# Performance work log

Hardware: AMD Instinct MI355X
Metric: run time of the kernel (lower is better)

Reference implementation:

```python
import jax, jax.numpy as jnp
import numpy as np
from jax import lax

B, IN_C, OUT_C, K, Z_DIM, H, W = 32, 128, 128, 3, 64, 96, 96
PAD = K // 2


def setup_inputs() -> dict:
    key = jax.random.key(0)
    k1, k2, k3, k4, k5, k6 = jax.random.split(key, 6)
    fan = (2.0 / (IN_C * K * K)) ** 0.5
    x = jax.random.normal(k1, (B, IN_C, H, W), dtype=jnp.float32)
    z = jax.random.normal(k2, (B, Z_DIM), dtype=jnp.float32)
    base_weight = jax.random.normal(k3, (OUT_C, IN_C, K, K), dtype=jnp.float32) * fan
    # torch nn.Linear weights are [out_features, in_features]
    gate_weight = jax.random.normal(k4, (OUT_C, Z_DIM), dtype=jnp.float32) * (1.0 / Z_DIM ** 0.5)
    pw_weight = jax.random.normal(k5, (OUT_C * IN_C, Z_DIM), dtype=jnp.float32) * (1.0 / Z_DIM ** 0.5)
    dw_weight = jax.random.normal(k6, (OUT_C * K * K, Z_DIM), dtype=jnp.float32) * (1.0 / Z_DIM ** 0.5)
    return {"x": x, "z": z, "base_weight": base_weight, "gate_weight": gate_weight,
            "pw_weight": pw_weight, "dw_weight": dw_weight}


def _merged_weight(z, base_weight, gate_weight, pw_weight, dw_weight):
    # BaseOp.get_weight: base * gate(z)  -> [B, out_c, in_c, k, k]
    gate = z @ gate_weight.T                       # [B, out_c]
    w_base = base_weight[None] * gate[:, :, None, None, None]
    # PWOp.get_weight (groups=1): [B, out_c, in_c, 1, 1]
    pw = (z @ pw_weight.T).reshape(B, OUT_C, IN_C)
    # DWOp.get_weight: [B, out_c, 1, k, k]
    dw = (z @ dw_weight.T).reshape(B, OUT_C, 1, K, K)
    # delta = pw * dw broadcast -> [B, out_c, in_c, k, k]
    delta = pw[:, :, :, None, None] * dw
    return w_base + delta


def _per_sample_conv(xi, wi):
    # xi: [in_c, H, W], wi: [out_c, in_c, k, k]
    return lax.conv_general_dilated(
        xi[None], wi, window_strides=(1, 1),
        padding=((PAD, PAD), (PAD, PAD)),
        dimension_numbers=("NCHW", "OIHW", "NCHW"))[0]


def reference(x, z, base_weight, gate_weight, pw_weight, dw_weight):
    w = _merged_weight(z, base_weight, gate_weight, pw_weight, dw_weight)
    return jax.vmap(_per_sample_conv)(x, w)  # [B, out_c, H, W]
```

## Files before the change

kernel.cpp:

```cpp
#include <hip/hip_runtime.h>
#include <hip/hip_bf16.h>

typedef __bf16 bf16x8 __attribute__((ext_vector_type(8)));
typedef float f32x4 __attribute__((ext_vector_type(4)));

__device__ __forceinline__ int swz(int n, int k) {
  int pair = n >> 1;
  int s = (((n & 1) << 2) | k) ^ (pair & 7);
  return (pair << 7) + (s << 4);
}

__device__ __forceinline__ void load_lds16(const void* g, void* l) {
  __builtin_amdgcn_global_load_lds((const __attribute__((address_space(1))) void*)g,
                                   (__attribute__((address_space(3))) void*)l, 16, 0, 0);
}

__global__ __launch_bounds__(512) void prep_kernel(
    const float* __restrict__ x, const float* __restrict__ z,
    const float* __restrict__ gw, const float* __restrict__ pww,
    const float* __restrict__ dww, const float* __restrict__ base,
    __hip_bfloat16* __restrict__ xn, __hip_bfloat16* __restrict__ Wt) {
  __shared__ float tile[128][97];
  int gid = blockIdx.x;
  int tid = threadIdx.x;

  if (gid < 3072) {
    int h = gid % 96;
    int b = gid / 96;
    const float* src = x + (size_t)b * 128 * 9216 + h * 96;
    for (int f = tid; f < 3072; f += 512) {
      int ic = f / 24, w4 = f - ic * 24;
      float4 v = *(const float4*)(src + (size_t)ic * 9216 + w4 * 4);
      tile[ic][w4 * 4 + 0] = v.x; tile[ic][w4 * 4 + 1] = v.y;
      tile[ic][w4 * 4 + 2] = v.z; tile[ic][w4 * 4 + 3] = v.w;
    }
    __syncthreads();
    __hip_bfloat16* bb  = xn + (size_t)b * 4 * 307328;
    __hip_bfloat16* dst = bb + (h + 1) * 3136 + 32;
    for (int o = tid; o < 1536; o += 512) {
      int grp = o / 384, rem = o - grp * 384;
      int w = rem >> 2, chunk = rem & 3;
      __hip_bfloat16 tmp[8];
      #pragma unroll
      for (int e = 0; e < 8; e++) tmp[e] = __float2bfloat16(tile[grp * 32 + chunk * 8 + e][w]);
      *(uint4*)(dst + (size_t)grp * 307328 + w * 32 + chunk * 8) = *(uint4*)tmp;
    }
    if (tid < 32) {
      int u = tid;
      int grp = u >> 3, rem = u & 7;
      int pw = (rem >> 2) ? 97 : 0, k = rem & 3;
      *(uint4*)(bb + (size_t)grp * 307328 + ((h + 1) * 98 + pw) * 32 + k * 8) = make_uint4(0, 0, 0, 0);
    }
    if (h == 0 || h == 95) {
      int ph = (h == 0) ? 0 : 97;
      for (int u = tid; u < 1568; u += 512) {
        int grp = u / 392, rem = u - grp * 392;
        int pw = rem >> 2, k = rem & 3;
        *(uint4*)(bb + (size_t)grp * 307328 + (ph * 98 + pw) * 32 + k * 8) = make_uint4(0, 0, 0, 0);
      }
    }
  } else {
    float* zs  = &tile[0][0];
    float (*res)[5] = (float (*)[5])(&tile[0][0] + 256);
    int pw = gid - 3072;
    int oc = pw & 127;
    int b0 = (pw >> 7) * 4;
    if (tid < 256) zs[tid] = z[b0 * 64 + tid];
    __syncthreads();
    int row = tid;
    if (row < 138) {
      const float* wrow = (row == 0) ? gw + (size_t)oc * 64
                        : (row < 10) ? dww + ((size_t)oc * 9 + (row - 1)) * 64
                                     : pww + ((size_t)oc * 128 + (row - 10)) * 64;
      float wr[64];
      #pragma unroll
      for (int i = 0; i < 16; i++) {
        float4 v = ((const float4*)wrow)[i];
        wr[4*i] = v.x; wr[4*i+1] = v.y; wr[4*i+2] = v.z; wr[4*i+3] = v.w;
      }
      #pragma unroll
      for (int bb = 0; bb < 4; bb++) {
        float a = 0.f;
        #pragma unroll
        for (int i = 0; i < 64; i++) a += zs[bb * 64 + i] * wr[i];
        res[row][bb] = a;
      }
    }
    __syncthreads();
    for (int e = tid; e < 2304; e += 512) {
      int icp = e & 15;
      int r1 = e >> 4;
      int tap = r1 % 9, gb = r1 / 9;
      int grp = gb & 3, bb = gb >> 2;
      int b = b0 + bb;
      int ic = grp * 32 + icp * 2;
      float g = res[0][bb], d = res[1 + tap][bb];
      float p0 = res[10 + ic][bb], p1 = res[11 + ic][bb];
      const float* bp = base + ((size_t)(oc * 128 + ic)) * 9 + tap;
      __hip_bfloat162 o2 = {__float2bfloat16(bp[0] * g + p0 * d),
                            __float2bfloat16(bp[9] * g + p1 * d)};
      *(__hip_bfloat162*)(Wt + ((((size_t)(b * 4 + grp)) * 9 + tap) * 128 + oc) * 32 + icp * 2) = o2;
    }
  }
}

__global__ __launch_bounds__(256, 3) void conv_kernel(
    const __hip_bfloat16* __restrict__ xn, const __hip_bfloat16* __restrict__ Wt,
    float* __restrict__ out) {
  __shared__ __align__(16) char smem[49152];
  char* const xt  = smem;
  char* const wb0 = smem + 24576;
  char* const wb1 = smem + 36864;

  int bid = blockIdx.x;
  int X = bid & 7, q = bid >> 3;
  int logical = X * 288 + q;
  int b   = logical / 72;
  int rem = logical - b * 72;
  int ocg = rem & 1;
  int t36 = rem >> 1;
  int hr  = t36 / 3;
  int wc  = t36 - hr * 3;
  int h0 = hr * 8, w0 = wc * 32;

  int tid = threadIdx.x;
  int lane = tid & 63, wid = tid >> 6;
  int l15 = lane & 15, lk = lane >> 4;

  int xoff[6];
  #pragma unroll
  for (int j = 0; j < 6; j++) {
    int p = j * 256 + tid; if (p > 1359) p = 1359;
    int pair = p >> 3, v = (p & 7) ^ (pair & 7);
    int n = (pair << 1) | (v >> 2), k = v & 3;
    int hh = n / 34, ww = n - hh * 34;
    xoff[j] = ((h0 + hh) * 98 + (w0 + ww)) * 32 + k * 8;
  }
  int wsoff[3];
  #pragma unroll
  for (int i = 0; i < 3; i++) {
    int p = i * 256 + tid;
    int pair = p >> 3, v = (p & 7) ^ (pair & 7);
    int n = (pair << 1) | (v >> 2), k = v & 3;
    int dx = n >> 6, ocl = n & 63;
    wsoff[i] = (dx * 128 + ocg * 64 + ocl) * 32 + k * 8;
  }

  const __hip_bfloat16* xbase = xn + (size_t)b * 4 * 307328;
  const __hip_bfloat16* wbase = Wt + (size_t)b * 147456;

  f32x4 acc[4][4];
  #pragma unroll
  for (int i = 0; i < 4; i++)
    #pragma unroll
    for (int j = 0; j < 4; j++) acc[i][j] = (f32x4){0.f, 0.f, 0.f, 0.f};

  #pragma unroll
  for (int i = 0; i < 3; i++)
    load_lds16(wbase + wsoff[i], wb0 + ((i * 256 + wid * 64) << 4));
  #pragma unroll
  for (int j = 0; j < 6; j++)
    load_lds16(xbase + xoff[j], xt + ((j * 256 + wid * 64) << 4));

#define PHASE(G, T, WCUR, WNXT, DOX, DOW, VM)                                      \
  {                                                                                \
    __builtin_amdgcn_s_barrier();                                                  \
    if (DOX) {                                                                     \
      const __hip_bfloat16* xsrc = xbase + (size_t)(G) * 307328;                   \
      _Pragma("unroll")                                                            \
      for (int j = 0; j < 6; j++)                                                  \
        load_lds16(xsrc + xoff[j], xt + ((j * 256 + wid * 64) << 4));              \
    }                                                                              \
    if (DOW) {                                                                     \
      const __hip_bfloat16* wsrc = wbase + (size_t)((G) * 9 + (T) * 3 + 3) * 4096; \
      _Pragma("unroll")                                                            \
      for (int i = 0; i < 3; i++)                                                  \
        load_lds16(wsrc + wsoff[i], (WNXT) + ((i * 256 + wid * 64) << 4));         \
    }                                                                              \
    asm volatile("s_waitcnt vmcnt(" #VM ")" ::: "memory");                         \
    __builtin_amdgcn_s_barrier();                                                  \
    _Pragma("unroll")                                                              \
    for (int dx = 0; dx < 3; dx++) {                                               \
      bf16x8 bfr[4], afr[4];                                                       \
      _Pragma("unroll")                                                            \
      for (int j = 0; j < 4; j++)                                                  \
        bfr[j] = *(const bf16x8*)((WCUR) + swz(dx * 64 + j * 16 + l15, lk));       \
      _Pragma("unroll")                                                            \
      for (int i = 0; i < 4; i++) {                                                \
        int r = wid * 2 + (i >> 1) + (T);                                          \
        int c = ((i & 1) << 4) + l15 + dx;                                         \
        afr[i] = *(const bf16x8*)(xt + swz(r * 34 + c, lk));                       \
      }                                                                            \
      _Pragma("unroll")                                                            \
      for (int i = 0; i < 4; i++)                                                  \
        _Pragma("unroll")                                                          \
        for (int j = 0; j < 4; j++)                                                \
          acc[i][j] = __builtin_amdgcn_mfma_f32_16x16x32_bf16(afr[i], bfr[j],      \
                                                              acc[i][j], 0, 0, 0); \
    }                                                                              \
  }

  PHASE(0, 0, wb0, wb1, 0, 1, 3)
  PHASE(0, 1, wb1, wb0, 0, 1, 3)
  PHASE(0, 2, wb0, wb1, 0, 1, 3)
  PHASE(1, 0, wb1, wb0, 1, 1, 3)
  PHASE(1, 1, wb0, wb1, 0, 1, 3)
  PHASE(1, 2, wb1, wb0, 0, 1, 3)
  PHASE(2, 0, wb0, wb1, 1, 1, 3)
  PHASE(2, 1, wb1, wb0, 0, 1, 3)
  PHASE(2, 2, wb0, wb1, 0, 1, 3)
  PHASE(3, 0, wb1, wb0, 1, 1, 3)
  PHASE(3, 1, wb0, wb1, 0, 1, 3)
  PHASE(3, 2, wb1, wb0, 0, 0, 0)
#undef PHASE

  float* ob = out + ((size_t)b * 128 + ocg * 64) * 9216;
  #pragma unroll
  for (int j = 0; j < 4; j++) {
    int oc = j * 16 + l15;
    float* op = ob + (size_t)oc * 9216 + h0 * 96 + w0 + lk * 4;
    #pragma unroll
    for (int i = 0; i < 4; i++) {
      int m0 = wid * 64 + i * 16;
      *(f32x4*)(op + (m0 >> 5) * 96 + (m0 & 31)) = acc[i][j];
    }
  }
}

extern "C" void kernel_launch(void* const* d_in, const int* in_sizes, int n_in,
                              void* d_out, int out_size, void* d_ws, size_t ws_size,
                              hipStream_t stream) {
  const float* x   = (const float*)d_in[0];
  const float* z   = (const float*)d_in[1];
  const float* bw  = (const float*)d_in[2];
  const float* gw  = (const float*)d_in[3];
  const float* pww = (const float*)d_in[4];
  const float* dww = (const float*)d_in[5];
  float* out = (float*)d_out;

  char* ws = (char*)d_ws;
  __hip_bfloat16* xn = (__hip_bfloat16*)ws;
  __hip_bfloat16* Wt = (__hip_bfloat16*)(ws + 78675968);

  hipLaunchKernelGGL(prep_kernel, dim3(4096), dim3(512), 0, stream,
                     x, z, gw, pww, dww, bw, xn, Wt);
  hipLaunchKernelGGL(conv_kernel, dim3(2304), dim3(256), 0, stream, xn, Wt, out);
}
```

Before: 138.9 us.

## Reorder conv taps by column to reuse input fragments across row taps

Changes the weight layout written by the prep kernel so that taps are ordered column-major (dx outer, dy inner). The conv kernel's per-phase inner loop now iterates over dy. It loads 8 input A-fragments once per phase and reuses them across the three row taps, instead of reloading 4 fragments for each of three column shifts (12 LDS reads down to 8 per phase). This costs more registers for the fragment array, which may pressure occupancy under the 3-blocks launch bound.

```diff
diff --git a/kernel.cpp b/kernel.cpp
--- a/kernel.cpp
+++ b/kernel.cpp
@@ -94,12 +94,13 @@
       int grp = gb & 3, bb = gb >> 2;
       int b = b0 + bb;
       int ic = grp * 32 + icp * 2;
+      int dy = tap / 3, dx = tap - dy * 3;
       float g = res[0][bb], d = res[1 + tap][bb];
       float p0 = res[10 + ic][bb], p1 = res[11 + ic][bb];
       const float* bp = base + ((size_t)(oc * 128 + ic)) * 9 + tap;
       __hip_bfloat162 o2 = {__float2bfloat16(bp[0] * g + p0 * d),
                             __float2bfloat16(bp[9] * g + p1 * d)};
-      *(__hip_bfloat162*)(Wt + ((((size_t)(b * 4 + grp)) * 9 + tap) * 128 + oc) * 32 + icp * 2) = o2;
+      *(__hip_bfloat162*)(Wt + ((((size_t)(b * 4 + grp)) * 9 + dx * 3 + dy) * 128 + oc) * 32 + icp * 2) = o2;
     }
   }
 }
@@ -142,8 +143,8 @@
     int p = i * 256 + tid;
     int pair = p >> 3, v = (p & 7) ^ (pair & 7);
     int n = (pair << 1) | (v >> 2), k = v & 3;
-    int dx = n >> 6, ocl = n & 63;
-    wsoff[i] = (dx * 128 + ocg * 64 + ocl) * 32 + k * 8;
+    int dy = n >> 6, ocl = n & 63;
+    wsoff[i] = (dy * 128 + ocg * 64 + ocl) * 32 + k * 8;
   }
 
   const __hip_bfloat16* xbase = xn + (size_t)b * 4 * 307328;
@@ -162,7 +163,7 @@
   for (int j = 0; j < 6; j++)
     load_lds16(xbase + xoff[j], xt + ((j * 256 + wid * 64) << 4));
 
-#define PHASE(G, T, WCUR, WNXT, DOX, DOW, VM)                                      \
+#define PHASE(G, DX, WCUR, WNXT, DOX, DOW, VM)                                     \
   {                                                                                \
     __builtin_amdgcn_s_barrier();                                                  \
     if (DOX) {                                                                     \
@@ -172,31 +173,32 @@
         load_lds16(xsrc + xoff[j], xt + ((j * 256 + wid * 64) << 4));              \
     }                                                                              \
     if (DOW) {                                                                     \
-      const __hip_bfloat16* wsrc = wbase + (size_t)((G) * 9 + (T) * 3 + 3) * 4096; \
+      const __hip_bfloat16* wsrc = wbase + (size_t)((G) * 9 + (DX) * 3 + 3) * 4096;\
       _Pragma("unroll")                                                            \
       for (int i = 0; i < 3; i++)                                                  \
         load_lds16(wsrc + wsoff[i], (WNXT) + ((i * 256 + wid * 64) << 4));         \
     }                                                                              \
     asm volatile("s_waitcnt vmcnt(" #VM ")" ::: "memory");                         \
     __builtin_amdgcn_s_barrier();                                                  \
+    bf16x8 afr[4][2];                                                              \
     _Pragma("unroll")                                                              \
-    for (int dx = 0; dx < 3; dx++) {                                               \
-      bf16x8 bfr[4], afr[4];                                                       \
+    for (int rr = 0; rr < 4; rr++)                                                 \
+      _Pragma("unroll")                                                            \
+      for (int cc = 0; cc < 2; cc++)                                               \
+        afr[rr][cc] = *(const bf16x8*)(xt +                                        \
+            swz((wid * 2 + rr) * 34 + cc * 16 + l15 + (DX), lk));                  \
+    _Pragma("unroll")                                                              \
+    for (int dy = 0; dy < 3; dy++) {                                               \
+      bf16x8 bfr[4];                                                               \
       _Pragma("unroll")                                                            \
       for (int j = 0; j < 4; j++)                                                  \
-        bfr[j] = *(const bf16x8*)((WCUR) + swz(dx * 64 + j * 16 + l15, lk));       \
-      _Pragma("unroll")                                                            \
-      for (int i = 0; i < 4; i++) {                                                \
-        int r = wid * 2 + (i >> 1) + (T);                                          \
-        int c = ((i & 1) << 4) + l15 + dx;                                         \
-        afr[i] = *(const bf16x8*)(xt + swz(r * 34 + c, lk));                       \
-      }                                                                            \
+        bfr[j] = *(const bf16x8*)((WCUR) + swz(dy * 64 + j * 16 + l15, lk));       \
       _Pragma("unroll")                                                            \
       for (int i = 0; i < 4; i++)                                                  \
         _Pragma("unroll")                                                          \
         for (int j = 0; j < 4; j++)                                                \
-          acc[i][j] = __builtin_amdgcn_mfma_f32_16x16x32_bf16(afr[i], bfr[j],      \
-                                                              acc[i][j], 0, 0, 0); \
+          acc[i][j] = __builtin_amdgcn_mfma_f32_16x16x32_bf16(                     \
+              afr[(i >> 1) + dy][i & 1], bfr[j], acc[i][j], 0, 0, 0);              \
     }                                                                              \
   }
 
```

Measured after the change: 137.2 us. About the same (-1.2%).
